# Kernel tuning notes

Hardware: AMD Instinct MI355X
Metric: run time of the kernel (lower is better)

The kernel has to match this reference:

```python
import jax, jax.numpy as jnp
import numpy as np

D_MODEL, D_K, D_V, N_HEADS = 1024, 64, 64, 16
BS, N_CTX = 2, 2048


def setup_inputs() -> dict:
    key = jax.random.key(0)
    ks = jax.random.split(key, 8)
    s = 0.02
    return {
        "x": jax.random.normal(ks[0], (BS, N_CTX, D_MODEL), dtype=jnp.float32),
        "Wq": jax.random.normal(ks[1], (D_K * N_HEADS, D_MODEL), dtype=jnp.float32) * s,
        "bq": jnp.zeros((D_K * N_HEADS,), dtype=jnp.float32),
        "Wk": jax.random.normal(ks[2], (D_K * N_HEADS, D_MODEL), dtype=jnp.float32) * s,
        "bk": jnp.zeros((D_K * N_HEADS,), dtype=jnp.float32),
        "Wv": jax.random.normal(ks[3], (D_V * N_HEADS, D_MODEL), dtype=jnp.float32) * s,
        "bv": jnp.zeros((D_V * N_HEADS,), dtype=jnp.float32),
        "Wo": jax.random.normal(ks[4], (D_MODEL, D_V * N_HEADS), dtype=jnp.float32) * s,
    }


def reference(x, Wq, bq, Wk, bk, Wv, bv, Wo):
    bs, n_ctx, d_model = x.shape
    # projections (torch Linear: y = x @ W.T + b)
    q = x @ Wq.T + bq  # (bs, n, H*dk)
    k = x @ Wk.T + bk
    v = x @ Wv.T + bv
    split = lambda t, d: t.reshape(bs, n_ctx, N_HEADS, d).transpose(0, 2, 1, 3)
    Q, K, V = split(q, D_K), split(k, D_K), split(v, D_V)  # (bs, H, n, d)
    scores = jnp.einsum('bhqd,bhkd->bhqk', Q / jnp.sqrt(jnp.float32(D_K)), K)
    # causal mask: x + (1 - 1/tril(ones)) == 0 on/below diag, -inf above
    causal = jnp.tril(jnp.ones((n_ctx, n_ctx), dtype=bool))
    scores = jnp.where(causal, scores, -jnp.inf)
    attn = jax.nn.softmax(scores, axis=-1)
    out = jnp.einsum('bhqk,bhkd->bhqd', attn, V)  # (bs, H, n, dv)
    out = out.transpose(0, 2, 1, 3).reshape(bs, n_ctx, N_HEADS * D_V)
    return out @ Wo.T  # no bias on output projection
```

## Files before the change

kernel.cpp:

```cpp
#include <hip/hip_runtime.h>
#include <hip/hip_bf16.h>


using bf16x8   = __attribute__((ext_vector_type(8))) __bf16;
using f32x4    = __attribute__((ext_vector_type(4))) float;
using ushort4v = __attribute__((ext_vector_type(4))) unsigned short;

__device__ __forceinline__ unsigned short f2bf(float f) {
    unsigned int u = __float_as_uint(f);
    u += 0x7FFFu + ((u >> 16) & 1u);
    return (unsigned short)(u >> 16);
}

__device__ __forceinline__ void gll16(const void* g, void* l) {
    __builtin_amdgcn_global_load_lds(
        (const __attribute__((address_space(1))) void*)g,
        (__attribute__((address_space(3))) void*)l, 16, 0, 0);
}

__global__ __launch_bounds__(256) void cast_bf16_kernel(
    const float* __restrict__ in, unsigned short* __restrict__ out, int n4) {
    int i = blockIdx.x * 256 + threadIdx.x;
    if (i >= n4) return;
    float4 f = reinterpret_cast<const float4*>(in)[i];
    ushort4v o;
    o.x = f2bf(f.x); o.y = f2bf(f.y); o.z = f2bf(f.z); o.w = f2bf(f.w);
    reinterpret_cast<ushort4v*>(out)[i] = o;
}

__global__ __launch_bounds__(256) void cast_w4_kernel(
    const float* __restrict__ w0, const float* __restrict__ w1,
    const float* __restrict__ w2, const float* __restrict__ w3,
    unsigned short* __restrict__ o0, unsigned short* __restrict__ o1,
    unsigned short* __restrict__ o2, unsigned short* __restrict__ o3) {
    const int z = blockIdx.y;
    const float* in = (z == 0) ? w0 : (z == 1) ? w1 : (z == 2) ? w2 : w3;
    unsigned short* out = (z == 0) ? o0 : (z == 1) ? o1 : (z == 2) ? o2 : o3;
    int i = blockIdx.x * 256 + threadIdx.x;
    float4 f = reinterpret_cast<const float4*>(in)[i];
    ushort4v o;
    o.x = f2bf(f.x); o.y = f2bf(f.y); o.z = f2bf(f.z); o.w = f2bf(f.w);
    reinterpret_cast<ushort4v*>(out)[i] = o;
}

__device__ __forceinline__ void gemm_core_128(
    const unsigned short* __restrict__ A, const unsigned short* __restrict__ B,
    int m0, int n0, int K,
    unsigned short* As, unsigned short* Bs, f32x4 acc[4][4]) {
    const int tid = threadIdx.x;
    const int lane = tid & 63;
    const int wid = tid >> 6;
    const int wr = wid >> 1, wc = wid & 1;
    const int l16 = lane & 15, lg = lane >> 4;

#pragma unroll
    for (int i = 0; i < 4; i++)
#pragma unroll
        for (int j = 0; j < 4; j++) acc[i][j] = f32x4{0.f, 0.f, 0.f, 0.f};

    const int srow = lane >> 2;
    const int scol = (lane & 3) * 8;
    const unsigned short* Ab0 = &A[(size_t)(m0 + wid * 16 + srow) * K + scol];
    const unsigned short* Ab1 = &A[(size_t)(m0 + 64 + wid * 16 + srow) * K + scol];
    const unsigned short* Bb0 = &B[(size_t)(n0 + wid * 16 + srow) * K + scol];
    const unsigned short* Bb1 = &B[(size_t)(n0 + 64 + wid * 16 + srow) * K + scol];
    unsigned short* AsW0 = As + (wid * 16) * 32;
    unsigned short* AsW1 = As + (64 + wid * 16) * 32;
    unsigned short* BsW0 = Bs + (wid * 16) * 32;
    unsigned short* BsW1 = Bs + (64 + wid * 16) * 32;

    for (int k0 = 0; k0 < K; k0 += 32) {
        __syncthreads();
        gll16(Ab0 + k0, AsW0);
        gll16(Ab1 + k0, AsW1);
        gll16(Bb0 + k0, BsW0);
        gll16(Bb1 + k0, BsW1);
        __syncthreads();
        bf16x8 af[4], bfr[4];
#pragma unroll
        for (int i = 0; i < 4; i++)
            af[i] = *reinterpret_cast<const bf16x8*>(&As[(64 * wr + 16 * i + l16) * 32 + 8 * lg]);
#pragma unroll
        for (int j = 0; j < 4; j++)
            bfr[j] = *reinterpret_cast<const bf16x8*>(&Bs[(64 * wc + 16 * j + l16) * 32 + 8 * lg]);
#pragma unroll
        for (int i = 0; i < 4; i++)
#pragma unroll
            for (int j = 0; j < 4; j++)
                acc[i][j] = __builtin_amdgcn_mfma_f32_16x16x32_bf16(af[i], bfr[j], acc[i][j], 0, 0, 0);
    }
}

__global__ __launch_bounds__(256) void gemm_qkv_kernel(
    const unsigned short* __restrict__ xbf,
    const unsigned short* __restrict__ wq, const unsigned short* __restrict__ wk,
    const unsigned short* __restrict__ wv,
    const float* __restrict__ bq, const float* __restrict__ bk, const float* __restrict__ bv,
    unsigned short* __restrict__ q_ws, unsigned short* __restrict__ k_ws,
    unsigned short* __restrict__ vt_ws) {
    __shared__ __align__(16) unsigned short As[128 * 32];
    __shared__ __align__(16) unsigned short Bs[128 * 32];
    const int z = blockIdx.z;
    const unsigned short* W = (z == 0) ? wq : ((z == 1) ? wk : wv);
    const float* bias = (z == 0) ? bq : ((z == 1) ? bk : bv);
    const float scale = (z == 0) ? 0.125f : 1.0f;
    const int m0 = blockIdx.y * 128;
    const int n0 = blockIdx.x * 128;

    f32x4 acc[4][4];
    gemm_core_128(xbf, W, m0, n0, 1024, As, Bs, acc);

    const int tid = threadIdx.x;
    const int lane = tid & 63;
    const int wid = tid >> 6;
    const int wr = wid >> 1, wc = wid & 1;
    const int l16 = lane & 15, lg = lane >> 4;

#pragma unroll
    for (int j = 0; j < 4; j++) {
        const int c = n0 + 64 * wc + 16 * j + l16;
        const float bc = bias[c];
        const int h = c >> 6, d = c & 63;
#pragma unroll
        for (int i = 0; i < 4; i++) {
            const int mb = m0 + 64 * wr + 16 * i + 4 * lg;
            if (z < 2) {
                unsigned short* dst = (z == 0) ? q_ws : k_ws;
#pragma unroll
                for (int r = 0; r < 4; r++) {
                    int m = mb + r;
                    int b = m >> 11, n = m & 2047;
                    float v = (acc[i][j][r] + bc) * scale;
                    dst[(((b * 16 + h) * 2048 + n) << 6) + d] = f2bf(v);
                }
            } else {
                int b = mb >> 11, n = mb & 2047;
                ushort4v pk;
                pk.x = f2bf(acc[i][j][0] + bc);
                pk.y = f2bf(acc[i][j][1] + bc);
                pk.z = f2bf(acc[i][j][2] + bc);
                pk.w = f2bf(acc[i][j][3] + bc);
                *reinterpret_cast<ushort4v*>(&vt_ws[((b * 16 + h) * 64 + d) * 2048 + n]) = pk;
            }
        }
    }
}

__global__ __launch_bounds__(256) void attn_kernel(
    const unsigned short* __restrict__ q_ws, const unsigned short* __restrict__ k_ws,
    const unsigned short* __restrict__ vt_ws, unsigned short* __restrict__ attn_out) {
    __shared__ __align__(16) unsigned short P_lds[4][2][16][40];
    const int tid = threadIdx.x;
    const int wid = tid >> 6, lane = tid & 63;
    const int l16 = lane & 15, lg = lane >> 4;
    const int gwid = blockIdx.x * 4 + wid;
    const int bh = gwid >> 6;
    const int p = gwid & 63;
    const int qA0 = p << 4;
    const int qB0 = 2032 - (p << 4);
    const unsigned short* qb = q_ws + bh * (2048 * 64);
    const unsigned short* kb = k_ws + bh * (2048 * 64);
    const unsigned short* vb = vt_ws + bh * (64 * 2048);

    bf16x8 aqA0 = *reinterpret_cast<const bf16x8*>(&qb[(qA0 + l16) * 64 + 8 * lg]);
    bf16x8 aqA1 = *reinterpret_cast<const bf16x8*>(&qb[(qA0 + l16) * 64 + 32 + 8 * lg]);
    bf16x8 aqB0 = *reinterpret_cast<const bf16x8*>(&qb[(qB0 + l16) * 64 + 8 * lg]);
    bf16x8 aqB1 = *reinterpret_cast<const bf16x8*>(&qb[(qB0 + l16) * 64 + 32 + 8 * lg]);

    f32x4 oA[4], oB[4];
#pragma unroll
    for (int j = 0; j < 4; j++) { oA[j] = f32x4{0.f, 0.f, 0.f, 0.f}; oB[j] = f32x4{0.f, 0.f, 0.f, 0.f}; }
    float mA = -1e30f, lA = 0.f, mB = -1e30f, lB = 0.f;

    bf16x8 k00 = *reinterpret_cast<const bf16x8*>(&kb[l16 * 64 + 8 * lg]);
    bf16x8 k01 = *reinterpret_cast<const bf16x8*>(&kb[l16 * 64 + 32 + 8 * lg]);
    bf16x8 k10 = *reinterpret_cast<const bf16x8*>(&kb[(16 + l16) * 64 + 8 * lg]);
    bf16x8 k11 = *reinterpret_cast<const bf16x8*>(&kb[(16 + l16) * 64 + 32 + 8 * lg]);

    const int kvEnd = qB0 + 16;
    for (int kv0 = 0; kv0 < kvEnd; kv0 += 32) {
        bf16x8 v0 = *reinterpret_cast<const bf16x8*>(&vb[l16 * 2048 + kv0 + 8 * lg]);
        bf16x8 v1 = *reinterpret_cast<const bf16x8*>(&vb[(16 + l16) * 2048 + kv0 + 8 * lg]);
        bf16x8 v2 = *reinterpret_cast<const bf16x8*>(&vb[(32 + l16) * 2048 + kv0 + 8 * lg]);
        bf16x8 v3 = *reinterpret_cast<const bf16x8*>(&vb[(48 + l16) * 2048 + kv0 + 8 * lg]);

        const f32x4 z = f32x4{0.f, 0.f, 0.f, 0.f};
        f32x4 sB0 = __builtin_amdgcn_mfma_f32_16x16x32_bf16(k00, aqB0, z, 0, 0, 0);
        sB0 = __builtin_amdgcn_mfma_f32_16x16x32_bf16(k01, aqB1, sB0, 0, 0, 0);
        f32x4 sB1 = __builtin_amdgcn_mfma_f32_16x16x32_bf16(k10, aqB0, z, 0, 0, 0);
        sB1 = __builtin_amdgcn_mfma_f32_16x16x32_bf16(k11, aqB1, sB1, 0, 0, 0);
        const bool actA = kv0 < qA0 + 16;
        f32x4 sA0 = z, sA1 = z;
        if (actA) {
            sA0 = __builtin_amdgcn_mfma_f32_16x16x32_bf16(k00, aqA0, z, 0, 0, 0);
            sA0 = __builtin_amdgcn_mfma_f32_16x16x32_bf16(k01, aqA1, sA0, 0, 0, 0);
            sA1 = __builtin_amdgcn_mfma_f32_16x16x32_bf16(k10, aqA0, z, 0, 0, 0);
            sA1 = __builtin_amdgcn_mfma_f32_16x16x32_bf16(k11, aqA1, sA1, 0, 0, 0);
        }
        if (kv0 + 32 < kvEnd) {
            const unsigned short* kr0 = &kb[(kv0 + 32 + l16) * 64 + 8 * lg];
            const unsigned short* kr1 = &kb[(kv0 + 48 + l16) * 64 + 8 * lg];
            k00 = *reinterpret_cast<const bf16x8*>(kr0);
            k01 = *reinterpret_cast<const bf16x8*>(kr0 + 32);
            k10 = *reinterpret_cast<const bf16x8*>(kr1);
            k11 = *reinterpret_cast<const bf16x8*>(kr1 + 32);
        }

        auto process = [&](f32x4 s0, f32x4 s1, int qX0, float& mX, float& lX,
                           f32x4* o, int slot) {
            const int kbase = kv0 + 4 * lg;
            const int qrow = qX0 + l16;
#pragma unroll
            for (int r = 0; r < 4; r++) {
                if (kbase + r > qrow) s0[r] = -1e30f;
                if (kbase + 16 + r > qrow) s1[r] = -1e30f;
            }
            float mx = fmaxf(fmaxf(fmaxf(s0[0], s0[1]), fmaxf(s0[2], s0[3])),
                             fmaxf(fmaxf(s1[0], s1[1]), fmaxf(s1[2], s1[3])));
            mx = fmaxf(mx, __shfl_xor(mx, 16));
            mx = fmaxf(mx, __shfl_xor(mx, 32));
            const float mnew = fmaxf(mX, mx);
            const float sf = __expf(mX - mnew);
            mX = mnew;
            float p0[4], p1[4];
#pragma unroll
            for (int r = 0; r < 4; r++) {
                p0[r] = __expf(s0[r] - mnew);
                p1[r] = __expf(s1[r] - mnew);
            }
            float sum = ((p0[0] + p0[1]) + (p0[2] + p0[3])) +
                        ((p1[0] + p1[1]) + (p1[2] + p1[3]));
            sum += __shfl_xor(sum, 16);
            sum += __shfl_xor(sum, 32);
            lX = lX * sf + sum;
            unsigned int a0 = (unsigned)f2bf(p0[0]) | ((unsigned)f2bf(p0[1]) << 16);
            unsigned int a1 = (unsigned)f2bf(p0[2]) | ((unsigned)f2bf(p0[3]) << 16);
            unsigned int b0 = (unsigned)f2bf(p1[0]) | ((unsigned)f2bf(p1[1]) << 16);
            unsigned int b1 = (unsigned)f2bf(p1[2]) | ((unsigned)f2bf(p1[3]) << 16);
            *reinterpret_cast<uint2*>(&P_lds[wid][slot][l16][4 * lg]) = make_uint2(a0, a1);
            *reinterpret_cast<uint2*>(&P_lds[wid][slot][l16][16 + 4 * lg]) = make_uint2(b0, b1);
            float sfT[4];
#pragma unroll
            for (int r = 0; r < 4; r++) sfT[r] = __shfl(sf, 4 * lg + r);
#pragma unroll
            for (int j = 0; j < 4; j++) {
                o[j][0] *= sfT[0]; o[j][1] *= sfT[1];
                o[j][2] *= sfT[2]; o[j][3] *= sfT[3];
            }
            bf16x8 pf = *reinterpret_cast<const bf16x8*>(&P_lds[wid][slot][l16][8 * lg]);
            o[0] = __builtin_amdgcn_mfma_f32_16x16x32_bf16(pf, v0, o[0], 0, 0, 0);
            o[1] = __builtin_amdgcn_mfma_f32_16x16x32_bf16(pf, v1, o[1], 0, 0, 0);
            o[2] = __builtin_amdgcn_mfma_f32_16x16x32_bf16(pf, v2, o[2], 0, 0, 0);
            o[3] = __builtin_amdgcn_mfma_f32_16x16x32_bf16(pf, v3, o[3], 0, 0, 0);
        };
        process(sB0, sB1, qB0, mB, lB, oB, 1);
        if (actA) process(sA0, sA1, qA0, mA, lA, oA, 0);
    }

    const int b = bh >> 4, h = bh & 15;
    auto epi = [&](int qX0, float lX, f32x4* o) {
        float inv[4];
#pragma unroll
        for (int r = 0; r < 4; r++) inv[r] = 1.0f / __shfl(lX, 4 * lg + r);
#pragma unroll
        for (int j = 0; j < 4; j++)
#pragma unroll
            for (int r = 0; r < 4; r++) {
                int n = qX0 + 4 * lg + r;
                attn_out[(size_t)(b * 2048 + n) * 1024 + h * 64 + 16 * j + l16] =
                    f2bf(o[j][r] * inv[r]);
            }
    };
    epi(qA0, lA, oA);
    epi(qB0, lB, oB);
}

__global__ __launch_bounds__(256) void gemm_out_kernel(
    const unsigned short* __restrict__ abf, const unsigned short* __restrict__ wo,
    float* __restrict__ out) {
    __shared__ __align__(16) unsigned short As[128 * 32];
    __shared__ __align__(16) unsigned short Bs[128 * 32];
    const int m0 = blockIdx.y * 128;
    const int n0 = blockIdx.x * 128;
    f32x4 acc[4][4];
    gemm_core_128(abf, wo, m0, n0, 1024, As, Bs, acc);

    const int tid = threadIdx.x;
    const int lane = tid & 63;
    const int wid = tid >> 6;
    const int wr = wid >> 1, wc = wid & 1;
    const int l16 = lane & 15, lg = lane >> 4;
#pragma unroll
    for (int j = 0; j < 4; j++) {
        const int c = n0 + 64 * wc + 16 * j + l16;
#pragma unroll
        for (int i = 0; i < 4; i++) {
#pragma unroll
            for (int r = 0; r < 4; r++) {
                int m = m0 + 64 * wr + 16 * i + 4 * lg + r;
                out[(size_t)m * 1024 + c] = acc[i][j][r];
            }
        }
    }
}

extern "C" void kernel_launch(void* const* d_in, const int* in_sizes, int n_in,
                              void* d_out, int out_size, void* d_ws, size_t ws_size,
                              hipStream_t stream) {
    const float* x  = (const float*)d_in[0];
    const float* Wq = (const float*)d_in[1];
    const float* bq = (const float*)d_in[2];
    const float* Wk = (const float*)d_in[3];
    const float* bk = (const float*)d_in[4];
    const float* Wv = (const float*)d_in[5];
    const float* bv = (const float*)d_in[6];
    const float* Wo = (const float*)d_in[7];
    float* out = (float*)d_out;

    char* ws = (char*)d_ws;
    unsigned short* xbf  = (unsigned short*)(ws);
    unsigned short* wqbf = (unsigned short*)(ws + (8u  << 20));
    unsigned short* wkbf = (unsigned short*)(ws + (10u << 20));
    unsigned short* wvbf = (unsigned short*)(ws + (12u << 20));
    unsigned short* wobf = (unsigned short*)(ws + (14u << 20));
    unsigned short* qws  = (unsigned short*)(ws + (16u << 20));
    unsigned short* kws  = (unsigned short*)(ws + (24u << 20));
    unsigned short* vtws = (unsigned short*)(ws + (32u << 20));
    unsigned short* aows = (unsigned short*)(ws + (40u << 20));

    cast_bf16_kernel<<<4096, 256, 0, stream>>>(x, xbf, 4096 * 1024 / 4);
    cast_w4_kernel<<<dim3(1024, 4), 256, 0, stream>>>(
        Wq, Wk, Wv, Wo, wqbf, wkbf, wvbf, wobf);

    gemm_qkv_kernel<<<dim3(8, 32, 3), 256, 0, stream>>>(
        xbf, wqbf, wkbf, wvbf, bq, bk, bv, qws, kws, vtws);

    attn_kernel<<<512, 256, 0, stream>>>(qws, kws, vtws, aows);

    gemm_out_kernel<<<dim3(8, 32, 1), 256, 0, stream>>>(aows, wobf, out);
}
```

Baseline: 281.1 us.

## Shrink GEMM tiles to 128x64 and streamline attention softmax with exp2 and lazy rescale

The projection and output GEMMs now use 128x64 tiles, doubling the grid so more blocks fill the GPU's compute units, at the cost of less reuse of each A tile. The attention softmax folds log2(e) into the Q scale so it can call exp2 directly. It applies the causal mask only on diagonal tiles and skips the O/l rescale unless the row max grows by more than 8. P is packed to bf16 with a hardware convert instruction. These changes cut per-tile VALU work in attention, but the lazy rescale lets probabilities grow to 2^8 before renormalisation, which relies on bf16 and fp32 headroom.

After: 274.1 us. 1.03x faster.

```diff
diff --git a/kernel.cpp b/kernel.cpp
--- a/kernel.cpp
+++ b/kernel.cpp
@@ -10,6 +10,12 @@
     unsigned int u = __float_as_uint(f);
     u += 0x7FFFu + ((u >> 16) & 1u);
     return (unsigned short)(u >> 16);
+}
+
+__device__ __forceinline__ unsigned cvtpk(float lo, float hi) {
+    unsigned r;
+    asm("v_cvt_pk_bf16_f32 %0, %1, %2" : "=v"(r) : "v"(lo), "v"(hi));
+    return r;
 }
 
 __device__ __forceinline__ void gll16(const void* g, void* l) {
@@ -43,10 +49,10 @@
     reinterpret_cast<ushort4v*>(out)[i] = o;
 }
 
-__device__ __forceinline__ void gemm_core_128(
+__device__ __forceinline__ void gemm_core_128x64(
     const unsigned short* __restrict__ A, const unsigned short* __restrict__ B,
     int m0, int n0, int K,
-    unsigned short* As, unsigned short* Bs, f32x4 acc[4][4]) {
+    unsigned short* As, unsigned short* Bs, f32x4 acc[4][2]) {
     const int tid = threadIdx.x;
     const int lane = tid & 63;
     const int wid = tid >> 6;
@@ -56,37 +62,34 @@
 #pragma unroll
     for (int i = 0; i < 4; i++)
 #pragma unroll
-        for (int j = 0; j < 4; j++) acc[i][j] = f32x4{0.f, 0.f, 0.f, 0.f};
+        for (int j = 0; j < 2; j++) acc[i][j] = f32x4{0.f, 0.f, 0.f, 0.f};
 
     const int srow = lane >> 2;
     const int scol = (lane & 3) * 8;
     const unsigned short* Ab0 = &A[(size_t)(m0 + wid * 16 + srow) * K + scol];
     const unsigned short* Ab1 = &A[(size_t)(m0 + 64 + wid * 16 + srow) * K + scol];
     const unsigned short* Bb0 = &B[(size_t)(n0 + wid * 16 + srow) * K + scol];
-    const unsigned short* Bb1 = &B[(size_t)(n0 + 64 + wid * 16 + srow) * K + scol];
     unsigned short* AsW0 = As + (wid * 16) * 32;
     unsigned short* AsW1 = As + (64 + wid * 16) * 32;
     unsigned short* BsW0 = Bs + (wid * 16) * 32;
-    unsigned short* BsW1 = Bs + (64 + wid * 16) * 32;
 
     for (int k0 = 0; k0 < K; k0 += 32) {
         __syncthreads();
         gll16(Ab0 + k0, AsW0);
         gll16(Ab1 + k0, AsW1);
         gll16(Bb0 + k0, BsW0);
-        gll16(Bb1 + k0, BsW1);
         __syncthreads();
-        bf16x8 af[4], bfr[4];
+        bf16x8 af[4], bfr[2];
 #pragma unroll
         for (int i = 0; i < 4; i++)
             af[i] = *reinterpret_cast<const bf16x8*>(&As[(64 * wr + 16 * i + l16) * 32 + 8 * lg]);
 #pragma unroll
-        for (int j = 0; j < 4; j++)
-            bfr[j] = *reinterpret_cast<const bf16x8*>(&Bs[(64 * wc + 16 * j + l16) * 32 + 8 * lg]);
+        for (int j = 0; j < 2; j++)
+            bfr[j] = *reinterpret_cast<const bf16x8*>(&Bs[(32 * wc + 16 * j + l16) * 32 + 8 * lg]);
 #pragma unroll
         for (int i = 0; i < 4; i++)
 #pragma unroll
-            for (int j = 0; j < 4; j++)
+            for (int j = 0; j < 2; j++)
                 acc[i][j] = __builtin_amdgcn_mfma_f32_16x16x32_bf16(af[i], bfr[j], acc[i][j], 0, 0, 0);
     }
 }
@@ -99,16 +102,16 @@
     unsigned short* __restrict__ q_ws, unsigned short* __restrict__ k_ws,
     unsigned short* __restrict__ vt_ws) {
     __shared__ __align__(16) unsigned short As[128 * 32];
-    __shared__ __align__(16) unsigned short Bs[128 * 32];
+    __shared__ __align__(16) unsigned short Bs[64 * 32];
     const int z = blockIdx.z;
     const unsigned short* W = (z == 0) ? wq : ((z == 1) ? wk : wv);
     const float* bias = (z == 0) ? bq : ((z == 1) ? bk : bv);
-    const float scale = (z == 0) ? 0.125f : 1.0f;
+    const float scale = (z == 0) ? 0.125f * 1.44269504f : 1.0f;
     const int m0 = blockIdx.y * 128;
-    const int n0 = blockIdx.x * 128;
-
-    f32x4 acc[4][4];
-    gemm_core_128(xbf, W, m0, n0, 1024, As, Bs, acc);
+    const int n0 = blockIdx.x * 64;
+
+    f32x4 acc[4][2];
+    gemm_core_128x64(xbf, W, m0, n0, 1024, As, Bs, acc);
 
     const int tid = threadIdx.x;
     const int lane = tid & 63;
@@ -117,8 +120,8 @@
     const int l16 = lane & 15, lg = lane >> 4;
 
 #pragma unroll
-    for (int j = 0; j < 4; j++) {
-        const int c = n0 + 64 * wc + 16 * j + l16;
+    for (int j = 0; j < 2; j++) {
+        const int c = n0 + 32 * wc + 16 * j + l16;
         const float bc = bias[c];
         const int h = c >> 6, d = c & 63;
 #pragma unroll
@@ -207,54 +210,61 @@
         }
 
         auto process = [&](f32x4 s0, f32x4 s1, int qX0, float& mX, float& lX,
-                           f32x4* o, int slot) {
-            const int kbase = kv0 + 4 * lg;
-            const int qrow = qX0 + l16;
-#pragma unroll
-            for (int r = 0; r < 4; r++) {
-                if (kbase + r > qrow) s0[r] = -1e30f;
-                if (kbase + 16 + r > qrow) s1[r] = -1e30f;
+                           f32x4* o, int slot, bool diag) {
+            if (diag) {
+                const int kbase = kv0 + 4 * lg;
+                const int qrow = qX0 + l16;
+#pragma unroll
+                for (int r = 0; r < 4; r++) {
+                    if (kbase + r > qrow) s0[r] = -1e30f;
+                    if (kbase + 16 + r > qrow) s1[r] = -1e30f;
+                }
             }
             float mx = fmaxf(fmaxf(fmaxf(s0[0], s0[1]), fmaxf(s0[2], s0[3])),
                              fmaxf(fmaxf(s1[0], s1[1]), fmaxf(s1[2], s1[3])));
             mx = fmaxf(mx, __shfl_xor(mx, 16));
             mx = fmaxf(mx, __shfl_xor(mx, 32));
-            const float mnew = fmaxf(mX, mx);
-            const float sf = __expf(mX - mnew);
-            mX = mnew;
+            if (!__all(mx <= mX + 8.0f)) {
+                const float mnew = fmaxf(mX, mx);
+                const float sf = __builtin_amdgcn_exp2f(mX - mnew);
+                mX = mnew;
+                lX *= sf;
+                float sfT[4];
+#pragma unroll
+                for (int r = 0; r < 4; r++) sfT[r] = __shfl(sf, 4 * lg + r);
+#pragma unroll
+                for (int j = 0; j < 4; j++) {
+                    o[j][0] *= sfT[0]; o[j][1] *= sfT[1];
+                    o[j][2] *= sfT[2]; o[j][3] *= sfT[3];
+                }
+            }
             float p0[4], p1[4];
 #pragma unroll
             for (int r = 0; r < 4; r++) {
-                p0[r] = __expf(s0[r] - mnew);
-                p1[r] = __expf(s1[r] - mnew);
+                p0[r] = __builtin_amdgcn_exp2f(s0[r] - mX);
+                p1[r] = __builtin_amdgcn_exp2f(s1[r] - mX);
             }
             float sum = ((p0[0] + p0[1]) + (p0[2] + p0[3])) +
                         ((p1[0] + p1[1]) + (p1[2] + p1[3]));
             sum += __shfl_xor(sum, 16);
             sum += __shfl_xor(sum, 32);
-            lX = lX * sf + sum;
-            unsigned int a0 = (unsigned)f2bf(p0[0]) | ((unsigned)f2bf(p0[1]) << 16);
-            unsigned int a1 = (unsigned)f2bf(p0[2]) | ((unsigned)f2bf(p0[3]) << 16);
-            unsigned int b0 = (unsigned)f2bf(p1[0]) | ((unsigned)f2bf(p1[1]) << 16);
-            unsigned int b1 = (unsigned)f2bf(p1[2]) | ((unsigned)f2bf(p1[3]) << 16);
-            *reinterpret_cast<uint2*>(&P_lds[wid][slot][l16][4 * lg]) = make_uint2(a0, a1);
-            *reinterpret_cast<uint2*>(&P_lds[wid][slot][l16][16 + 4 * lg]) = make_uint2(b0, b1);
-            float sfT[4];
-#pragma unroll
-            for (int r = 0; r < 4; r++) sfT[r] = __shfl(sf, 4 * lg + r);
-#pragma unroll
-            for (int j = 0; j < 4; j++) {
-                o[j][0] *= sfT[0]; o[j][1] *= sfT[1];
-                o[j][2] *= sfT[2]; o[j][3] *= sfT[3];
-            }
+            lX += sum;
+            uint2 w0 = make_uint2(cvtpk(p0[0], p0[1]), cvtpk(p0[2], p0[3]));
+            uint2 w1 = make_uint2(cvtpk(p1[0], p1[1]), cvtpk(p1[2], p1[3]));
+            *reinterpret_cast<uint2*>(&P_lds[wid][slot][l16][4 * lg]) = w0;
+            *reinterpret_cast<uint2*>(&P_lds[wid][slot][l16][16 + 4 * lg]) = w1;
             bf16x8 pf = *reinterpret_cast<const bf16x8*>(&P_lds[wid][slot][l16][8 * lg]);
             o[0] = __builtin_amdgcn_mfma_f32_16x16x32_bf16(pf, v0, o[0], 0, 0, 0);
             o[1] = __builtin_amdgcn_mfma_f32_16x16x32_bf16(pf, v1, o[1], 0, 0, 0);
             o[2] = __builtin_amdgcn_mfma_f32_16x16x32_bf16(pf, v2, o[2], 0, 0, 0);
             o[3] = __builtin_amdgcn_mfma_f32_16x16x32_bf16(pf, v3, o[3], 0, 0, 0);
         };
-        process(sB0, sB1, qB0, mB, lB, oB, 1);
-        if (actA) process(sA0, sA1, qA0, mA, lA, oA, 0);
+        const bool diagB = (kv0 + 32 >= kvEnd);
+        process(sB0, sB1, qB0, mB, lB, oB, 1, diagB);
+        if (actA) {
+            const bool diagA = (kv0 + 32 >= qA0 + 16);
+            process(sA0, sA1, qA0, mA, lA, oA, 0, diagA);
+        }
     }
 
     const int b = bh >> 4, h = bh & 15;
@@ -279,11 +289,11 @@
     const unsigned short* __restrict__ abf, const unsigned short* __restrict__ wo,
     float* __restrict__ out) {
     __shared__ __align__(16) unsigned short As[128 * 32];
-    __shared__ __align__(16) unsigned short Bs[128 * 32];
+    __shared__ __align__(16) unsigned short Bs[64 * 32];
     const int m0 = blockIdx.y * 128;
-    const int n0 = blockIdx.x * 128;
-    f32x4 acc[4][4];
-    gemm_core_128(abf, wo, m0, n0, 1024, As, Bs, acc);
+    const int n0 = blockIdx.x * 64;
+    f32x4 acc[4][2];
+    gemm_core_128x64(abf, wo, m0, n0, 1024, As, Bs, acc);
 
     const int tid = threadIdx.x;
     const int lane = tid & 63;
@@ -291,8 +301,8 @@
     const int wr = wid >> 1, wc = wid & 1;
     const int l16 = lane & 15, lg = lane >> 4;
 #pragma unroll
-    for (int j = 0; j < 4; j++) {
-        const int c = n0 + 64 * wc + 16 * j + l16;
+    for (int j = 0; j < 2; j++) {
+        const int c = n0 + 32 * wc + 16 * j + l16;
 #pragma unroll
         for (int i = 0; i < 4; i++) {
 #pragma unroll
@@ -332,10 +342,10 @@
     cast_w4_kernel<<<dim3(1024, 4), 256, 0, stream>>>(
         Wq, Wk, Wv, Wo, wqbf, wkbf, wvbf, wobf);
 
-    gemm_qkv_kernel<<<dim3(8, 32, 3), 256, 0, stream>>>(
+    gemm_qkv_kernel<<<dim3(16, 32, 3), 256, 0, stream>>>(
         xbf, wqbf, wkbf, wvbf, bq, bk, bv, qws, kws, vtws);
 
     attn_kernel<<<512, 256, 0, stream>>>(qws, kws, vtws, aows);
 
-    gemm_out_kernel<<<dim3(8, 32, 1), 256, 0, stream>>>(aows, wobf, out);
-}
+    gemm_out_kernel<<<dim3(16, 32), 256, 0, stream>>>(aows, wobf, out);
+}
```
